# Performance work log

Measured on AMD Instinct MI355X. Metric: run time of the kernel, lower is better.

Reference implementation:

```python
import jax, jax.numpy as jnp
import numpy as np

TOPK = 2

def setup_inputs() -> dict:
    key = jax.random.key(0)
    ks = jax.random.split(key, 5)
    B, S, D, H, E = 2, 4096, 1024, 2048, 8
    x = jax.random.normal(ks[0], (B, S, D), dtype=jnp.float32)
    router_w = jax.random.normal(ks[1], (E, D), dtype=jnp.float32) * 0.02
    w1 = jax.random.normal(ks[2], (E, D, H), dtype=jnp.float32) * 0.02
    w3 = jax.random.normal(ks[3], (E, D, H), dtype=jnp.float32) * 0.02
    w2 = jax.random.normal(ks[4], (E, H, D), dtype=jnp.float32) * 0.02
    return {"x": x, "router_w": router_w, "w1": w1, "w3": w3, "w2": w2}

def reference(x, router_w, w1, w3, w2):
    B, S, D = x.shape
    E = router_w.shape[0]
    xf = x.reshape(-1, D)                      # [T, D]
    T = xf.shape[0]
    logits = (xf @ router_w.T).astype(jnp.float32)      # [T, E]
    weights, indices = jax.lax.top_k(logits, TOPK)      # [T, k]
    weights = jax.nn.softmax(weights, axis=-1).astype(x.dtype)
    prob = jax.nn.softmax(logits, axis=-1)              # [T, E] fp32
    P = prob.mean(axis=0).astype(x.dtype)               # [E]
    mask = jnp.zeros((T, E), jnp.float32).at[jnp.arange(T)[:, None], indices].set(1.0)
    f = mask.mean(axis=0).astype(x.dtype)               # [E]
    aux_loss = E * jnp.sum(f * P)
    out = jnp.zeros_like(xf)
    for e in range(E):
        # combine weight for expert e per token (0 if not routed here)
        coef = jnp.sum(jnp.where(indices == e, weights, jnp.zeros_like(weights)), axis=-1)  # [T]
        h = jax.nn.silu(xf @ w1[e]) * (xf @ w3[e])      # [T, H] SwiGLU
        out = out + coef[:, None] * (h @ w2[e])         # masked combine == gather/scatter
    return out.reshape(B, S, D), aux_loss
```

## Files before the change

### kernel.cpp

```cpp
#include <hip/hip_runtime.h>
#include <hip/hip_bf16.h>

#define TT 8192
#define DD 1024
#define HH 2048
#define EE 8

typedef __bf16 bf16x8 __attribute__((ext_vector_type(8)));
typedef float floatx4 __attribute__((ext_vector_type(4)));
typedef short shortx8 __attribute__((ext_vector_type(8)));

__device__ __forceinline__ short f2bf(float f) {
  unsigned u = __float_as_uint(f);
  u += 0x7fffu + ((u >> 16) & 1u);
  return (short)(u >> 16);
}

__device__ __forceinline__ void gld16(const void* g, void* l) {
  __builtin_amdgcn_global_load_lds((const __attribute__((address_space(1))) void*)g,
                                   (__attribute__((address_space(3))) void*)l, 16, 0, 0);
}

__global__ __launch_bounds__(256) void router_kernel(
    const float* __restrict__ x, const float* __restrict__ rw,
    int* __restrict__ cpad, float* __restrict__ ppad,
    int* __restrict__ list_token, float* __restrict__ list_coef,
    short* __restrict__ xb)
{
  __shared__ int   sE0[32], sE1[32], lcnt[EE], sbase[EE], lp0[32], lp1[32];
  __shared__ float sG0[32], sG1[32], sP[EE];
  const int tid = threadIdx.x;
  if (tid < EE) { sP[tid] = 0.f; lcnt[tid] = 0; }
  __syncthreads();
  const int lane = tid & 63, wv = tid >> 6;
  const int t0 = blockIdx.x * 32;
  for (int ti = 0; ti < 8; ++ti) {
    const int s = wv * 8 + ti;
    const int t = t0 + s;
    float sc[EE];
#pragma unroll
    for (int e = 0; e < EE; ++e) sc[e] = 0.f;
#pragma unroll
    for (int j = 0; j < 4; ++j) {
      float4 xv = *(const float4*)(x + (size_t)t * DD + j * 256 + lane * 4);
#pragma unroll
      for (int e = 0; e < EE; ++e) {
        float4 rv = *(const float4*)(rw + e * DD + j * 256 + lane * 4);
        sc[e] += xv.x * rv.x + xv.y * rv.y + xv.z * rv.z + xv.w * rv.w;
      }
      if (xb) {
        short4 sv = make_short4(f2bf(xv.x), f2bf(xv.y), f2bf(xv.z), f2bf(xv.w));
        *(short4*)(xb + (size_t)t * DD + j * 256 + lane * 4) = sv;
      }
    }
#pragma unroll
    for (int off = 32; off > 0; off >>= 1)
#pragma unroll
      for (int e = 0; e < EE; ++e)
        sc[e] += __shfl_down(sc[e], off);
    if (lane == 0) {
      int i0 = 0; float l0 = sc[0];
      for (int e = 1; e < EE; ++e) if (sc[e] > l0) { l0 = sc[e]; i0 = e; }
      int i1 = -1; float l1 = -3.4e38f;
      for (int e = 0; e < EE; ++e) if (e != i0 && sc[e] > l1) { l1 = sc[e]; i1 = e; }
      const float g0 = 1.f / (1.f + __expf(l1 - l0));
      float pr[EE]; float sum = 0.f;
      for (int e = 0; e < EE; ++e) { pr[e] = __expf(sc[e] - l0); sum += pr[e]; }
      const float inv = 1.f / sum;
      for (int e = 0; e < EE; ++e) atomicAdd(&sP[e], pr[e] * inv);
      sE0[s] = i0; sE1[s] = i1; sG0[s] = g0; sG1[s] = 1.f - g0;
    }
  }
  __syncthreads();
  if (tid < 32) {
    lp0[tid] = atomicAdd(&lcnt[sE0[tid]], 1);
    lp1[tid] = atomicAdd(&lcnt[sE1[tid]], 1);
  }
  __syncthreads();
  if (tid < EE) {
    sbase[tid] = atomicAdd(&cpad[tid * 16], lcnt[tid]);
    atomicAdd(&ppad[tid * 16], sP[tid]);
  }
  __syncthreads();
  if (tid < 32) {
    int e0 = sE0[tid], e1 = sE1[tid], t = t0 + tid;
    int p0 = sbase[e0] + lp0[tid];
    int p1 = sbase[e1] + lp1[tid];
    list_token[e0 * TT + p0] = t; list_coef[e0 * TT + p0] = sG0[tid];
    list_token[e1 * TT + p1] = t; list_coef[e1 * TT + p1] = sG1[tid];
  }
}

__global__ void aux_kernel(const int* __restrict__ cpad, const float* __restrict__ ppad,
                           int* __restrict__ offsets, float* __restrict__ out_aux)
{
  if (threadIdx.x == 0) {
    float aux = 0.f; int off = 0;
    for (int e = 0; e < EE; ++e) {
      aux += ((float)cpad[e * 16] / (float)TT) * (ppad[e * 16] / (float)TT);
      offsets[e] = off; off += cpad[e * 16];
    }
    *out_aux = aux * (float)EE;
  }
}

__global__ __launch_bounds__(256) void convt_kernel(const float* __restrict__ in, short* __restrict__ out,
                                                    int R, int C, int mode)
{
  __shared__ short T[64 * 74];
  const int t = threadIdx.x;
  in  += (size_t)blockIdx.z * R * C;
  out += (size_t)blockIdx.z * R * C * (mode ? 2 : 1);
  const int c0 = blockIdx.x * 64, r0 = blockIdx.y * 64;
#pragma unroll
  for (int p = 0; p < 4; ++p) {
    int r = p * 16 + (t >> 4), c4 = (t & 15) * 4;
    float4 v = *(const float4*)(in + (size_t)(r0 + r) * C + c0 + c4);
    short4 s = make_short4(f2bf(v.x), f2bf(v.y), f2bf(v.z), f2bf(v.w));
    *(short4*)&T[r * 74 + c4] = s;
  }
  __syncthreads();
#pragma unroll
  for (int q = 0; q < 2; ++q) {
    int u = q * 256 + t;
    int oc = u >> 3, k8 = (u & 7) * 8;
    shortx8 s;
#pragma unroll
    for (int j = 0; j < 8; ++j) s[j] = T[(k8 + j) * 74 + oc];
    int c = c0 + oc;
    int grow = (mode == 0) ? c : (2 * (c & ~31) + (c & 31) + ((mode == 2) ? 32 : 0));
    *(shortx8*)&out[(size_t)grow * R + r0 + k8] = s;
  }
}


#define PH_BAR()  { __builtin_amdgcn_s_barrier(); __builtin_amdgcn_sched_barrier(0); }
#define WAITL0()  { asm volatile("s_waitcnt lgkmcnt(0)" ::: "memory"); __builtin_amdgcn_sched_barrier(0); }
#define WAITVN(n) { asm volatile("s_waitcnt vmcnt(" #n ")" ::: "memory"); __builtin_amdgcn_sched_barrier(0); }

template<int NT>
__device__ __forceinline__ void mma_core(char* SM, int tid,
    const char* a00, const char* a01, const char* a10, const char* a11,
    const char* b00, const char* b01, const char* b10, const char* b11,
    floatx4 (&acc)[8][4])
{
  const int lane = tid & 63, w = tid >> 6;
  const int l16 = lane & 15, quad = lane >> 4;
  const int wm = (w >> 2) & 1, wn = w & 3;
  const int cx = (((l16 >> 1) & 1) << 4) | (((l16 >> 2) & 1) << 5) | ((l16 & 1) << 6);
  const int ck0 = (quad * 16) ^ cx;
  const int arb = (wm * 128 + l16) * 128;
  const int brb = 32768 + (wn * 64 + l16) * 128;
  const int wq = w * 2048;

#define SA_(u,h,p0,p1) { gld16((p0) + (size_t)(u) * 128, SM + (((u) & 1) << 16) + (h) * 16384 + wq); \
                         gld16((p1) + (size_t)(u) * 128, SM + (((u) & 1) << 16) + (h) * 16384 + wq + 1024); }
#define SB_(u,h,p0,p1) { gld16((p0) + (size_t)(u) * 128, SM + (((u) & 1) << 16) + 32768 + (h) * 16384 + wq); \
                         gld16((p1) + (size_t)(u) * 128, SM + (((u) & 1) << 16) + 32768 + (h) * 16384 + wq + 1024); }
#define LA_(mi) { a[mi][0] = *(const bf16x8*)(SM + cur + arb + (mi) * 2048 + ck0); \
                  a[mi][1] = *(const bf16x8*)(SM + cur + arb + (mi) * 2048 + (ck0 ^ 64)); }
#define LB_(ni) { b[ni][0] = *(const bf16x8*)(SM + cur + brb + (ni) * 2048 + ck0); \
                  b[ni][1] = *(const bf16x8*)(SM + cur + brb + (ni) * 2048 + (ck0 ^ 64)); }
#define MM_(mi,ni) { acc[mi][ni] = __builtin_amdgcn_mfma_f32_16x16x32_bf16(a[mi][0], b[ni][0], acc[mi][ni], 0, 0, 0); \
                     acc[mi][ni] = __builtin_amdgcn_mfma_f32_16x16x32_bf16(a[mi][1], b[ni][1], acc[mi][ni], 0, 0, 0); }

  SA_(0, 0, a00, a01); SA_(0, 1, a10, a11);
  SB_(0, 0, b00, b01); SB_(0, 1, b10, b11);
  SA_(1, 0, a00, a01); SA_(1, 1, a10, a11);
  WAITVN(4);
  __builtin_amdgcn_s_barrier();
  __builtin_amdgcn_sched_barrier(0);

#pragma unroll 2
  for (int t = 0; t < NT; ++t) {
    const int cur = (t & 1) << 16;
    bf16x8 a[8][2], b[4][2];
    LA_(0) LA_(1) LA_(2) LA_(3) LB_(0) LB_(1)
    if (t + 1 < NT) SB_(t + 1, 0, b00, b01);
    PH_BAR(); WAITL0();
    __builtin_amdgcn_s_setprio(1);
    MM_(0,0) MM_(1,0) MM_(2,0) MM_(3,0) MM_(0,1) MM_(1,1) MM_(2,1) MM_(3,1)
    __builtin_amdgcn_s_setprio(0);
    PH_BAR();
    LA_(4) LA_(5) LA_(6) LA_(7) LB_(2) LB_(3)
    if (t + 1 < NT) SB_(t + 1, 1, b10, b11);
    PH_BAR(); WAITL0();
    __builtin_amdgcn_s_setprio(1);
    MM_(4,2) MM_(5,2) MM_(6,2) MM_(7,2) MM_(4,3) MM_(5,3) MM_(6,3) MM_(7,3)
    __builtin_amdgcn_s_setprio(0);
    PH_BAR();
    if (t + 2 < NT) SA_(t + 2, 0, a00, a01);
    PH_BAR();
    __builtin_amdgcn_s_setprio(1);
    MM_(0,2) MM_(1,2) MM_(2,2) MM_(3,2) MM_(0,3) MM_(1,3) MM_(2,3) MM_(3,3)
    __builtin_amdgcn_s_setprio(0);
    PH_BAR();
    if (t + 2 < NT) SA_(t + 2, 1, a10, a11);
    PH_BAR();
    __builtin_amdgcn_s_setprio(1);
    MM_(4,0) MM_(5,0) MM_(6,0) MM_(7,0) MM_(4,1) MM_(5,1) MM_(6,1) MM_(7,1)
    __builtin_amdgcn_s_setprio(0);
    if (t + 2 < NT) { WAITVN(4); } else { WAITVN(0); }
    PH_BAR();
  }
#undef SA_
#undef SB_
#undef LA_
#undef LB_
#undef MM_
}

__global__ __launch_bounds__(512, 2) void g1p_kernel(
    const short* __restrict__ xb, const short* __restrict__ w13t,
    const int* __restrict__ cpad, const int* __restrict__ offsets,
    const int* __restrict__ list_token, short* __restrict__ Hbuf)
{
  const int lin = blockIdx.x + 16 * (blockIdx.y + 32 * blockIdx.z);
  const int xcd = lin & 7, c = lin >> 3;
  const int e = c >> 6, rb = (c >> 1) & 31, nb = (xcd << 1) | (c & 1);
  const int cnt = cpad[e * 16];
  if (rb * 256 >= cnt) return;
  __shared__ char SM[131072];
  const int tid = threadIdx.x;
  const int lane = tid & 63, w = tid >> 6;
  const int srow = lane >> 3;
  const int scol = (((lane ^ (lane >> 4)) & 1) << 4)
                 | ((((lane >> 1) ^ (lane >> 5)) & 1) << 5)
                 | ((((lane >> 2) ^ (lane >> 3)) & 1) << 6);
  const int* lt = list_token + e * TT;
  const char* ap[2][2];
#pragma unroll
  for (int h = 0; h < 2; ++h)
#pragma unroll
    for (int i = 0; i < 2; ++i) {
      int gr = rb * 256 + h * 128 + (w * 2 + i) * 8 + srow;
      int tok = (gr < cnt) ? lt[gr] : lt[0];
      ap[h][i] = (const char*)xb + (size_t)tok * 2048 + scol;
    }
  const char* bb = (const char*)w13t + ((size_t)e * 4096 + nb * 256) * 2048
                 + (size_t)(w * 16 + srow) * 2048 + scol;
  floatx4 acc[8][4] = {};
  mma_core<16>(SM, tid, ap[0][0], ap[0][1], ap[1][0], ap[1][1],
               bb, bb + 8 * 2048, bb + 128 * 2048, bb + 136 * 2048, acc);
  const int off = offsets[e];
  const int l16 = lane & 15, quad = lane >> 4;
  const int wm = (w >> 2) & 1, wn = w & 3;
#pragma unroll
  for (int mi = 0; mi < 8; ++mi)
#pragma unroll
    for (int r = 0; r < 4; ++r) {
      int grow = rb * 256 + wm * 128 + mi * 16 + quad * 4 + r;
      if (grow < cnt) {
        size_t rowbase = (size_t)(off + grow) * HH + nb * 128 + wn * 32;
#pragma unroll
        for (int ni = 0; ni < 2; ++ni) {
          float aa = acc[mi][ni][r], bbv = acc[mi][ni + 2][r];
          float hv = aa / (1.f + __expf(-aa)) * bbv;
          Hbuf[rowbase + ni * 16 + l16] = f2bf(hv);
        }
      }
    }
}

__global__ __launch_bounds__(256, 2) void g2x_kernel(
    const short* __restrict__ Hbuf, const short* __restrict__ w2t,
    const int* __restrict__ cpad, const int* __restrict__ offsets,
    const int* __restrict__ list_token, const float* __restrict__ list_coef,
    float* __restrict__ out)
{
  const int lin = blockIdx.x + 8 * (blockIdx.y + 64 * blockIdx.z);
  const int xcd = lin & 7, c = lin >> 3;
  const int nb = xcd, e = c >> 6, rb = c & 63;
  const int cnt = cpad[e * 16];
  if (rb * 128 >= cnt) return;
  __shared__ short Asm[128 * 32];
  __shared__ short Bsm[128 * 32];
  const int tid = threadIdx.x, lane = tid & 63, wv = tid >> 6;
  const int wm = (wv >> 1) * 64, wn = (wv & 1) * 64;
  const int quad = lane >> 4, l16 = lane & 15;
  floatx4 acc[4][4] = {{{0.f}}};
  const int off = offsets[e];
  const int qrow = wv * 32 + (lane >> 2);
  const int qcb = (lane & 3) * 16;
  const char* ag = (const char*)(Hbuf + (size_t)(off + rb * 128 + qrow) * HH) + qcb;
  const char* bg = (const char*)(w2t + (size_t)e * DD * HH + (size_t)(nb * 128 + qrow) * HH) + qcb;
  char* al = (char*)Asm + wv * 2048;
  char* bl = (char*)Bsm + wv * 2048;
  int aro[4], bro[4];
#pragma unroll
  for (int mi = 0; mi < 4; ++mi) aro[mi] = (wm + mi * 16 + l16) * 32 + quad * 8;
#pragma unroll
  for (int ni = 0; ni < 4; ++ni) bro[ni] = (wn + ni * 16 + l16) * 32 + quad * 8;

  for (int k0 = 0; k0 < HH; k0 += 32) {
    __syncthreads();
    gld16(ag + (size_t)k0 * 2, al);
    gld16(ag + (size_t)k0 * 2 + 16 * HH * 2, al + 1024);
    gld16(bg + (size_t)k0 * 2, bl);
    gld16(bg + (size_t)k0 * 2 + 16 * HH * 2, bl + 1024);
    __syncthreads();
    bf16x8 af[4], bf[4];
#pragma unroll
    for (int mi = 0; mi < 4; ++mi) af[mi] = *(const bf16x8*)&Asm[aro[mi]];
#pragma unroll
    for (int ni = 0; ni < 4; ++ni) bf[ni] = *(const bf16x8*)&Bsm[bro[ni]];
#pragma unroll
    for (int mi = 0; mi < 4; ++mi)
#pragma unroll
      for (int ni = 0; ni < 4; ++ni)
        acc[mi][ni] = __builtin_amdgcn_mfma_f32_16x16x32_bf16(af[mi], bf[ni], acc[mi][ni], 0, 0, 0);
  }
#pragma unroll
  for (int mi = 0; mi < 4; ++mi)
#pragma unroll
    for (int r = 0; r < 4; ++r) {
      int row = wm + mi * 16 + quad * 4 + r;
      int grow = rb * 128 + row;
      if (grow < cnt) {
        int tokid = list_token[e * TT + grow];
        float coef = list_coef[e * TT + grow];
        float* orow = out + (size_t)tokid * DD + (size_t)nb * 128 + wn;
#pragma unroll
        for (int ni = 0; ni < 4; ++ni)
          atomicAdd(&orow[ni * 16 + l16], coef * acc[mi][ni][r]);
      }
    }
}

__global__ __launch_bounds__(256, 2) void g1s_kernel(
    const float* __restrict__ x, const float* __restrict__ w1, const float* __restrict__ w3,
    const int* __restrict__ cpad, const int* __restrict__ offsets,
    const int* __restrict__ list_token, short* __restrict__ Hbuf)
{
  const int e = blockIdx.z, rb = blockIdx.y, nb = blockIdx.x;
  const int cnt = cpad[e * 16];
  if (rb * 128 >= cnt) return;
  __shared__ short Asm[128 * 40];
  __shared__ short B1sm[128 * 40];
  __shared__ short B3sm[128 * 40];
  const int tid = threadIdx.x, lane = tid & 63, wv = tid >> 6;
  const int wm = (wv >> 1) * 64, wn = (wv & 1) * 64;
  const int quad = lane >> 4, l16 = lane & 15;
  floatx4 acc1[4][4] = {{{0.f}}};
  floatx4 acc3[4][4] = {{{0.f}}};
  const int ar = tid >> 3, ak = (tid & 7) * 4;
  const int bp = tid & 63, bq = tid >> 6;
  const int bswz = (bq ^ ((bp >> 2) & 3)) * 8;
  const int bo0 = (2 * bp) * 40 + bswz, bo1 = bo0 + 40;
  int aro[4], bro[4];
#pragma unroll
  for (int mi = 0; mi < 4; ++mi) aro[mi] = (wm + mi * 16 + l16) * 40 + quad * 8;
#pragma unroll
  for (int ni = 0; ni < 4; ++ni) {
    int nl = wn + ni * 16 + l16;
    bro[ni] = nl * 40 + ((quad ^ ((nl >> 3) & 3)) * 8);
  }
  int tok[4];
#pragma unroll
  for (int i = 0; i < 4; ++i) {
    int gr = rb * 128 + ar + 32 * i;
    tok[i] = (gr < cnt) ? list_token[e * TT + gr] : list_token[e * TT];
  }
  const float* w1e = w1 + (size_t)e * DD * HH + (size_t)nb * 128;
  const float* w3e = w3 + (size_t)e * DD * HH + (size_t)nb * 128;
  for (int k0 = 0; k0 < DD; k0 += 32) {
    __syncthreads();
#pragma unroll
    for (int i = 0; i < 4; ++i) {
      int r = ar + 32 * i;
      float4 v = *(const float4*)(x + (size_t)tok[i] * DD + k0 + ak);
      short4 sv = make_short4(f2bf(v.x), f2bf(v.y), f2bf(v.z), f2bf(v.w));
      *(short4*)&Asm[r * 40 + ak] = sv;
    }
    {
      float2 u[8];
#pragma unroll
      for (int j = 0; j < 8; ++j) u[j] = *(const float2*)(w1e + (size_t)(k0 + bq * 8 + j) * HH + 2 * bp);
      shortx8 p0, p1;
#pragma unroll
      for (int j = 0; j < 8; ++j) { p0[j] = f2bf(u[j].x); p1[j] = f2bf(u[j].y); }
      *(shortx8*)&B1sm[bo0] = p0; *(shortx8*)&B1sm[bo1] = p1;
    }
    {
      float2 u[8];
#pragma unroll
      for (int j = 0; j < 8; ++j) u[j] = *(const float2*)(w3e + (size_t)(k0 + bq * 8 + j) * HH + 2 * bp);
      shortx8 p0, p1;
#pragma unroll
      for (int j = 0; j < 8; ++j) { p0[j] = f2bf(u[j].x); p1[j] = f2bf(u[j].y); }
      *(shortx8*)&B3sm[bo0] = p0; *(shortx8*)&B3sm[bo1] = p1;
    }
    __syncthreads();
    bf16x8 af[4], b1f[4], b3f[4];
#pragma unroll
    for (int mi = 0; mi < 4; ++mi) af[mi] = *(const bf16x8*)&Asm[aro[mi]];
#pragma unroll
    for (int ni = 0; ni < 4; ++ni) {
      b1f[ni] = *(const bf16x8*)&B1sm[bro[ni]];
      b3f[ni] = *(const bf16x8*)&B3sm[bro[ni]];
    }
#pragma unroll
    for (int mi = 0; mi < 4; ++mi)
#pragma unroll
      for (int ni = 0; ni < 4; ++ni) {
        acc1[mi][ni] = __builtin_amdgcn_mfma_f32_16x16x32_bf16(af[mi], b1f[ni], acc1[mi][ni], 0, 0, 0);
        acc3[mi][ni] = __builtin_amdgcn_mfma_f32_16x16x32_bf16(af[mi], b3f[ni], acc3[mi][ni], 0, 0, 0);
      }
  }
  const int off = offsets[e];
#pragma unroll
  for (int mi = 0; mi < 4; ++mi)
#pragma unroll
    for (int r = 0; r < 4; ++r) {
      int row = wm + mi * 16 + quad * 4 + r;
      int grow = rb * 128 + row;
      if (grow < cnt) {
        size_t rowbase = (size_t)(off + grow) * HH + (size_t)nb * 128 + wn;
#pragma unroll
        for (int ni = 0; ni < 4; ++ni) {
          float a = acc1[mi][ni][r], b = acc3[mi][ni][r];
          float h = a / (1.f + __expf(-a)) * b;
          Hbuf[rowbase + ni * 16 + l16] = f2bf(h);
        }
      }
    }
}

__global__ __launch_bounds__(256, 2) void g2s_kernel(
    const short* __restrict__ Hbuf, const float* __restrict__ w2,
    const int* __restrict__ cpad, const int* __restrict__ offsets,
    const int* __restrict__ list_token, const float* __restrict__ list_coef,
    float* __restrict__ out)
{
  const int e = blockIdx.z, rb = blockIdx.y, nb = blockIdx.x;
  const int cnt = cpad[e * 16];
  if (rb * 128 >= cnt) return;
  __shared__ short Asm[128 * 40];
  __shared__ short Bsm[128 * 40];
  const int tid = threadIdx.x, lane = tid & 63, wv = tid >> 6;
  const int wm = (wv >> 1) * 64, wn = (wv & 1) * 64;
  const int quad = lane >> 4, l16 = lane & 15;
  floatx4 acc[4][4] = {{{0.f}}};
  const int ar = tid >> 3, ak = (tid & 7) * 4;
  const int bp = tid & 63, bq = tid >> 6;
  const int bswz = (bq ^ ((bp >> 2) & 3)) * 8;
  const int bo0 = (2 * bp) * 40 + bswz, bo1 = bo0 + 40;
  int aro[4], bro[4];
#pragma unroll
  for (int mi = 0; mi < 4; ++mi) aro[mi] = (wm + mi * 16 + l16) * 40 + quad * 8;
#pragma unroll
  for (int ni = 0; ni < 4; ++ni) {
    int nl = wn + ni * 16 + l16;
    bro[ni] = nl * 40 + ((quad ^ ((nl >> 3) & 3)) * 8);
  }
  const int off = offsets[e];
  size_t hrow[4];
#pragma unroll
  for (int i = 0; i < 4; ++i) {
    int gr = rb * 128 + ar + 32 * i;
    int cg = (gr < cnt) ? gr : (cnt - 1);
    hrow[i] = (size_t)(off + cg) * HH;
  }
  const float* w2e = w2 + (size_t)e * HH * DD + (size_t)nb * 128;
  for (int k0 = 0; k0 < HH; k0 += 32) {
    __syncthreads();
#pragma unroll
    for (int i = 0; i < 4; ++i) {
      int r = ar + 32 * i;
      short4 sv = *(const short4*)(Hbuf + hrow[i] + k0 + ak);
      *(short4*)&Asm[r * 40 + ak] = sv;
    }
    {
      float2 u[8];
#pragma unroll
      for (int j = 0; j < 8; ++j) u[j] = *(const float2*)(w2e + (size_t)(k0 + bq * 8 + j) * DD + 2 * bp);
      shortx8 p0, p1;
#pragma unroll
      for (int j = 0; j < 8; ++j) { p0[j] = f2bf(u[j].x); p1[j] = f2bf(u[j].y); }
      *(shortx8*)&Bsm[bo0] = p0; *(shortx8*)&Bsm[bo1] = p1;
    }
    __syncthreads();
    bf16x8 af[4], bf[4];
#pragma unroll
    for (int mi = 0; mi < 4; ++mi) af[mi] = *(const bf16x8*)&Asm[aro[mi]];
#pragma unroll
    for (int ni = 0; ni < 4; ++ni) bf[ni] = *(const bf16x8*)&Bsm[bro[ni]];
#pragma unroll
    for (int mi = 0; mi < 4; ++mi)
#pragma unroll
      for (int ni = 0; ni < 4; ++ni)
        acc[mi][ni] = __builtin_amdgcn_mfma_f32_16x16x32_bf16(af[mi], bf[ni], acc[mi][ni], 0, 0, 0);
  }
#pragma unroll
  for (int mi = 0; mi < 4; ++mi)
#pragma unroll
    for (int r = 0; r < 4; ++r) {
      int row = wm + mi * 16 + quad * 4 + r;
      int grow = rb * 128 + row;
      if (grow < cnt) {
        int tokid = list_token[e * TT + grow];
        float coef = list_coef[e * TT + grow];
        float* orow = out + (size_t)tokid * DD + (size_t)nb * 128 + wn;
#pragma unroll
        for (int ni = 0; ni < 4; ++ni)
          atomicAdd(&orow[ni * 16 + l16], coef * acc[mi][ni][r]);
      }
    }
}

extern "C" void kernel_launch(void* const* d_in, const int* in_sizes, int n_in,
                              void* d_out, int out_size, void* d_ws, size_t ws_size,
                              hipStream_t stream)
{
  const float* x  = (const float*)d_in[0];
  const float* rw = (const float*)d_in[1];
  const float* w1 = (const float*)d_in[2];
  const float* w3 = (const float*)d_in[3];
  const float* w2 = (const float*)d_in[4];
  float* out = (float*)d_out;

  char* ws = (char*)d_ws;
  int*   cpad      = (int*)(ws + 0);
  float* ppad      = (float*)(ws + 512);
  int*   offsets   = (int*)(ws + 1024);
  int*   list_tok  = (int*)(ws + 4096);
  float* list_coef = (float*)(ws + 4096 + EE * TT * 4);

  const size_t OFF_W1T = 1u << 20;
  const size_t OFF_W3T = OFF_W1T + ((size_t)EE * DD * HH * 2);
  const size_t OFF_XBF = OFF_W3T + ((size_t)EE * DD * HH * 2);
  const size_t OFF_HB  = OFF_XBF + ((size_t)TT * DD * 2);
  const size_t NEED    = OFF_HB + ((size_t)(2 * TT + 128) * HH * 2);

  hipMemsetAsync(ws, 0, 1024, stream);
  hipMemsetAsync(d_out, 0, (size_t)TT * DD * sizeof(float), stream);

  const bool fast = (ws_size >= NEED);
  short* XBF = fast ? (short*)(ws + OFF_XBF) : nullptr;

  router_kernel<<<256, 256, 0, stream>>>(x, rw, cpad, ppad, list_tok, list_coef, XBF);
  aux_kernel<<<1, 64, 0, stream>>>(cpad, ppad, offsets, out + (size_t)TT * DD);

  if (fast) {
    short* W13T = (short*)(ws + OFF_W1T);
    short* HB   = (short*)(ws + OFF_HB);
    convt_kernel<<<dim3(HH / 64, DD / 64, EE), 256, 0, stream>>>(w1, W13T, DD, HH, 1);
    convt_kernel<<<dim3(HH / 64, DD / 64, EE), 256, 0, stream>>>(w3, W13T, DD, HH, 2);
    g1p_kernel<<<dim3(16, 32, EE), 512, 0, stream>>>(XBF, W13T, cpad, offsets, list_tok, HB);
    convt_kernel<<<dim3(DD / 64, HH / 64, EE), 256, 0, stream>>>(w2, W13T, HH, DD, 0);
    g2x_kernel<<<dim3(8, 64, EE), 256, 0, stream>>>(HB, W13T, cpad, offsets, list_tok, list_coef, out);
  } else {
    short* HB = (short*)(ws + (1 << 20));
    g1s_kernel<<<dim3(HH / 128, TT / 128, EE), 256, 0, stream>>>(x, w1, w3, cpad, offsets, list_tok, HB);
    g2s_kernel<<<dim3(DD / 128, TT / 128, EE), 256, 0, stream>>>(HB, w2, cpad, offsets, list_tok, list_coef, out);
  }
}
```

Before: 607.7 us.

## Replace atomic scatter in down-proj with bf16 staging buffer and combine kernel

The down-projection GEMM now writes its per-slot results as bf16 into a staging buffer instead of doing float atomicAdds into the output. A new combine kernel reads each token's two expert rows and writes the weighted sum directly, which also removes the output memset. The router records per-token packed (expert, slot) indices for this gather. The w1/w3 conversion launches are merged into one kernel, and w2 goes to a separate buffer. The change adds a kernel launch and an extra pass over intermediate data, and it rounds expert outputs to bf16 before the combine.

```diff
diff --git a/kernel.cpp b/kernel.cpp
--- a/kernel.cpp
+++ b/kernel.cpp
@@ -16,6 +16,10 @@
   return (short)(u >> 16);
 }
 
+__device__ __forceinline__ float bf2f(short s) {
+  return __uint_as_float(((unsigned)(unsigned short)s) << 16);
+}
+
 __device__ __forceinline__ void gld16(const void* g, void* l) {
   __builtin_amdgcn_global_load_lds((const __attribute__((address_space(1))) void*)g,
                                    (__attribute__((address_space(3))) void*)l, 16, 0, 0);
@@ -25,6 +29,7 @@
     const float* __restrict__ x, const float* __restrict__ rw,
     int* __restrict__ cpad, float* __restrict__ ppad,
     int* __restrict__ list_token, float* __restrict__ list_coef,
+    int* __restrict__ tokpk, float* __restrict__ tokcf,
     short* __restrict__ xb)
 {
   __shared__ int   sE0[32], sE1[32], lcnt[EE], sbase[EE], lp0[32], lp1[32];
@@ -88,6 +93,8 @@
     int p1 = sbase[e1] + lp1[tid];
     list_token[e0 * TT + p0] = t; list_coef[e0 * TT + p0] = sG0[tid];
     list_token[e1 * TT + p1] = t; list_coef[e1 * TT + p1] = sG1[tid];
+    tokpk[t * 2]     = (e0 << 13) | p0;  tokcf[t * 2]     = sG0[tid];
+    tokpk[t * 2 + 1] = (e1 << 13) | p1;  tokcf[t * 2 + 1] = sG1[tid];
   }
 }
 
@@ -104,13 +111,46 @@
   }
 }
 
+__global__ __launch_bounds__(256) void convt13_kernel(const float* __restrict__ w1,
+                                                      const float* __restrict__ w3,
+                                                      short* __restrict__ out)
+{
+  __shared__ short T[64 * 74];
+  const int t = threadIdx.x;
+  const int z = blockIdx.z;
+  const int is3 = (z >= EE) ? 1 : 0;
+  const int e = is3 ? (z - EE) : z;
+  const float* in = (is3 ? w3 : w1) + (size_t)e * DD * HH;
+  short* o = out + (size_t)e * DD * HH * 2;
+  const int c0 = blockIdx.x * 64, r0 = blockIdx.y * 64;
+#pragma unroll
+  for (int p = 0; p < 4; ++p) {
+    int r = p * 16 + (t >> 4), c4 = (t & 15) * 4;
+    float4 v = *(const float4*)(in + (size_t)(r0 + r) * HH + c0 + c4);
+    short4 s = make_short4(f2bf(v.x), f2bf(v.y), f2bf(v.z), f2bf(v.w));
+    *(short4*)&T[r * 74 + c4] = s;
+  }
+  __syncthreads();
+#pragma unroll
+  for (int q = 0; q < 2; ++q) {
+    int u = q * 256 + t;
+    int oc = u >> 3, k8 = (u & 7) * 8;
+    shortx8 s;
+#pragma unroll
+    for (int j = 0; j < 8; ++j) s[j] = T[(k8 + j) * 74 + oc];
+    int c = c0 + oc;
+    int grow = 2 * (c & ~31) + (c & 31) + (is3 ? 32 : 0);
+    *(shortx8*)&o[(size_t)grow * DD + r0 + k8] = s;
+  }
+}
+
 __global__ __launch_bounds__(256) void convt_kernel(const float* __restrict__ in, short* __restrict__ out,
-                                                    int R, int C, int mode)
+                                                    int R, int C)
 {
   __shared__ short T[64 * 74];
   const int t = threadIdx.x;
   in  += (size_t)blockIdx.z * R * C;
-  out += (size_t)blockIdx.z * R * C * (mode ? 2 : 1);
+  out += (size_t)blockIdx.z * R * C;
   const int c0 = blockIdx.x * 64, r0 = blockIdx.y * 64;
 #pragma unroll
   for (int p = 0; p < 4; ++p) {
@@ -127,9 +167,7 @@
     shortx8 s;
 #pragma unroll
     for (int j = 0; j < 8; ++j) s[j] = T[(k8 + j) * 74 + oc];
-    int c = c0 + oc;
-    int grow = (mode == 0) ? c : (2 * (c & ~31) + (c & 31) + ((mode == 2) ? 32 : 0));
-    *(shortx8*)&out[(size_t)grow * R + r0 + k8] = s;
+    *(shortx8*)&out[(size_t)(c0 + oc) * R + r0 + k8] = s;
   }
 }
 
@@ -262,11 +300,10 @@
     }
 }
 
-__global__ __launch_bounds__(256, 2) void g2x_kernel(
+__global__ __launch_bounds__(256, 2) void g2o_kernel(
     const short* __restrict__ Hbuf, const short* __restrict__ w2t,
     const int* __restrict__ cpad, const int* __restrict__ offsets,
-    const int* __restrict__ list_token, const float* __restrict__ list_coef,
-    float* __restrict__ out)
+    short* __restrict__ Obuf)
 {
   const int lin = blockIdx.x + 8 * (blockIdx.y + 64 * blockIdx.z);
   const int xcd = lin & 7, c = lin >> 3;
@@ -317,14 +354,37 @@
       int row = wm + mi * 16 + quad * 4 + r;
       int grow = rb * 128 + row;
       if (grow < cnt) {
-        int tokid = list_token[e * TT + grow];
-        float coef = list_coef[e * TT + grow];
-        float* orow = out + (size_t)tokid * DD + (size_t)nb * 128 + wn;
+        short* orow = Obuf + (size_t)(off + grow) * DD + nb * 128 + wn;
 #pragma unroll
         for (int ni = 0; ni < 4; ++ni)
-          atomicAdd(&orow[ni * 16 + l16], coef * acc[mi][ni][r]);
+          orow[ni * 16 + l16] = f2bf(acc[mi][ni][r]);
       }
     }
+}
+
+__global__ __launch_bounds__(256) void combine_kernel(
+    const short* __restrict__ Obuf, const int* __restrict__ offsets,
+    const int* __restrict__ tokpk, const float* __restrict__ tokcf,
+    float* __restrict__ out)
+{
+  const int tid = threadIdx.x, lane = tid & 63, wv = tid >> 6;
+  const int t = blockIdx.x * 4 + wv;
+  const int pk0 = tokpk[t * 2], pk1 = tokpk[t * 2 + 1];
+  const float c0 = tokcf[t * 2], c1 = tokcf[t * 2 + 1];
+  const size_t r0 = (size_t)(offsets[pk0 >> 13] + (pk0 & 8191)) * DD;
+  const size_t r1 = (size_t)(offsets[pk1 >> 13] + (pk1 & 8191)) * DD;
+  float* orow = out + (size_t)t * DD;
+#pragma unroll
+  for (int p = 0; p < 2; ++p) {
+    int cidx = p * 512 + lane * 8;
+    shortx8 a = *(const shortx8*)(Obuf + r0 + cidx);
+    shortx8 b = *(const shortx8*)(Obuf + r1 + cidx);
+    float v[8];
+#pragma unroll
+    for (int j = 0; j < 8; ++j) v[j] = c0 * bf2f(a[j]) + c1 * bf2f(b[j]);
+    *(float4*)(orow + cidx)     = make_float4(v[0], v[1], v[2], v[3]);
+    *(float4*)(orow + cidx + 4) = make_float4(v[4], v[5], v[6], v[7]);
+  }
 }
 
 __global__ __launch_bounds__(256, 2) void g1s_kernel(
@@ -525,6 +585,8 @@
   int*   offsets   = (int*)(ws + 1024);
   int*   list_tok  = (int*)(ws + 4096);
   float* list_coef = (float*)(ws + 4096 + EE * TT * 4);
+  int*   tokpk     = (int*)(ws + 4096 + 2 * EE * TT * 4);
+  float* tokcf     = (float*)(ws + 4096 + 2 * EE * TT * 4 + 2 * TT * 4);
 
   const size_t OFF_W1T = 1u << 20;
   const size_t OFF_W3T = OFF_W1T + ((size_t)EE * DD * HH * 2);
@@ -533,23 +595,25 @@
   const size_t NEED    = OFF_HB + ((size_t)(2 * TT + 128) * HH * 2);
 
   hipMemsetAsync(ws, 0, 1024, stream);
-  hipMemsetAsync(d_out, 0, (size_t)TT * DD * sizeof(float), stream);
 
   const bool fast = (ws_size >= NEED);
   short* XBF = fast ? (short*)(ws + OFF_XBF) : nullptr;
 
-  router_kernel<<<256, 256, 0, stream>>>(x, rw, cpad, ppad, list_tok, list_coef, XBF);
+  router_kernel<<<256, 256, 0, stream>>>(x, rw, cpad, ppad, list_tok, list_coef, tokpk, tokcf, XBF);
   aux_kernel<<<1, 64, 0, stream>>>(cpad, ppad, offsets, out + (size_t)TT * DD);
 
   if (fast) {
     short* W13T = (short*)(ws + OFF_W1T);
+    short* OB   = (short*)(ws + OFF_W1T);
+    short* W2T  = (short*)(ws + OFF_W3T);
     short* HB   = (short*)(ws + OFF_HB);
-    convt_kernel<<<dim3(HH / 64, DD / 64, EE), 256, 0, stream>>>(w1, W13T, DD, HH, 1);
-    convt_kernel<<<dim3(HH / 64, DD / 64, EE), 256, 0, stream>>>(w3, W13T, DD, HH, 2);
+    convt13_kernel<<<dim3(HH / 64, DD / 64, 2 * EE), 256, 0, stream>>>(w1, w3, W13T);
     g1p_kernel<<<dim3(16, 32, EE), 512, 0, stream>>>(XBF, W13T, cpad, offsets, list_tok, HB);
-    convt_kernel<<<dim3(DD / 64, HH / 64, EE), 256, 0, stream>>>(w2, W13T, HH, DD, 0);
-    g2x_kernel<<<dim3(8, 64, EE), 256, 0, stream>>>(HB, W13T, cpad, offsets, list_tok, list_coef, out);
+    convt_kernel<<<dim3(DD / 64, HH / 64, EE), 256, 0, stream>>>(w2, W2T, HH, DD);
+    g2o_kernel<<<dim3(8, 64, EE), 256, 0, stream>>>(HB, W2T, cpad, offsets, OB);
+    combine_kernel<<<TT / 4, 256, 0, stream>>>(OB, offsets, tokpk, tokcf, out);
   } else {
+    hipMemsetAsync(d_out, 0, (size_t)TT * DD * sizeof(float), stream);
     short* HB = (short*)(ws + (1 << 20));
     g1s_kernel<<<dim3(HH / 128, TT / 128, EE), 256, 0, stream>>>(x, w1, w3, cpad, offsets, list_tok, HB);
     g2s_kernel<<<dim3(DD / 128, TT / 128, EE), 256, 0, stream>>>(HB, w2, cpad, offsets, list_tok, list_coef, out);
```

Result: faster. 587.2 us (-3.4%).
